# Performance work log

Hardware: AMD Instinct MI355X
Metric: run time of the kernel (lower is better)

The kernel has to match this reference:

```python
import jax, jax.numpy as jnp
import numpy as np

N = 50000        # nodes
E = 800000       # edges (avg degree 16)
IN = 128         # n_feat
C0, H0 = 32, 4   # layer0: out_channels, heads (concat -> 128)
C1, H1 = 32, 1   # layer1: out_channels, heads (mean)
NEG_SLOPE = 0.2


def setup_inputs() -> dict:
    key = jax.random.key(0)
    ks = jax.random.split(key, 16)
    def p(k, shape, fan):
        return jax.random.normal(k, shape, jnp.float32) / np.float32(np.sqrt(fan))
    x = jax.random.normal(ks[0], (N, IN), jnp.float32)
    edge_index = jax.random.randint(ks[1], (2, E), 0, N, dtype=jnp.int32)
    return {
        "x": x,
        "edge_index": edge_index,
        # layer 0 GATConv: in=128 -> 4 heads x 32, concat
        "W0": p(ks[2], (H0 * C0, IN), IN),
        "att_src0": p(ks[3], (H0, C0), C0),
        "att_dst0": p(ks[4], (H0, C0), C0),
        "bias0": jnp.zeros((H0 * C0,), jnp.float32),
        "linW0": p(ks[5], (H0 * C0, IN), IN),
        "linb0": jnp.zeros((H0 * C0,), jnp.float32),
        # layer 1 GATConv: in=128 -> 1 head x 32, mean
        "W1": p(ks[6], (H1 * C1, H0 * C0), H0 * C0),
        "att_src1": p(ks[7], (H1, C1), C1),
        "att_dst1": p(ks[8], (H1, C1), C1),
        "bias1": jnp.zeros((C1,), jnp.float32),
        "linW1": p(ks[9], (C1, H0 * C0), H0 * C0),
        "linb1": jnp.zeros((C1,), jnp.float32),
    }


def gat_conv(x, src, dst, W, att_src, att_dst, bias, concat):
    """PyG-style GATConv (self-loops already appended to src/dst)."""
    n = x.shape[0]
    H, C = att_src.shape
    h = (x @ W.T).reshape(n, H, C)                       # [N,H,C]
    a_src = jnp.einsum('nhc,hc->nh', h, att_src)          # [N,H]
    a_dst = jnp.einsum('nhc,hc->nh', h, att_dst)          # [N,H]
    e = jax.nn.leaky_relu(a_src[src] + a_dst[dst], NEG_SLOPE)  # [E,H]
    # segment softmax over incoming edges of each dst node
    m = jax.ops.segment_max(e, dst, num_segments=n)       # [N,H]
    ex = jnp.exp(e - m[dst])
    denom = jax.ops.segment_sum(ex, dst, num_segments=n)  # [N,H]
    alpha = ex / (denom[dst] + 1e-16)                     # [E,H]
    out = jax.ops.segment_sum(h[src] * alpha[:, :, None], dst, num_segments=n)  # [N,H,C]
    out = out.reshape(n, H * C) if concat else out.mean(axis=1)
    return out + bias


def reference(x, edge_index, W0, att_src0, att_dst0, bias0, linW0, linb0,
              W1, att_src1, att_dst1, bias1, linW1, linb1):
    n = x.shape[0]
    loop = jnp.arange(n, dtype=edge_index.dtype)
    src = jnp.concatenate([edge_index[0], loop])  # add self-loops
    dst = jnp.concatenate([edge_index[1], loop])
    # layer 0: conv + linear skip, then ELU (eval mode -> dropout is a no-op)
    h = gat_conv(x, src, dst, W0, att_src0, att_dst0, bias0, True) + x @ linW0.T + linb0
    h = jax.nn.elu(h)
    # layer 1 (last): conv + linear skip, no activation
    out = gat_conv(h, src, dst, W1, att_src1, att_dst1, bias1, False) + h @ linW1.T + linb1
    return out
```

## Files before the change

kernel.cpp:

```cpp
#include <hip/hip_runtime.h>
#include <hip/hip_bf16.h>


typedef __attribute__((ext_vector_type(8))) short bf8_t;
typedef __attribute__((ext_vector_type(4))) float f4_t;

#define NBUCK 256
#define BCAP  8192

__device__ inline short f2bf(float f) {
    return (short)__builtin_bit_cast(unsigned short, __float2bfloat16(f));
}
__device__ inline float blo(unsigned int p) { return __uint_as_float(p << 16); }
__device__ inline float bhi(unsigned int p) { return __uint_as_float(p & 0xffff0000u); }
__device__ inline float lrexp(float e) {
    e = (e > 0.f) ? e : 0.2f * e;
    return __expf(e);
}

__global__ void k_gz(int* __restrict__ gcur) {
    gcur[threadIdx.x] = threadIdx.x * BCAP;
}

__global__ __launch_bounds__(256) void k_initbucket(
    const int* __restrict__ ei,
    const float* __restrict__ W0, const float* __restrict__ lW0,
    const float* __restrict__ W1, const float* __restrict__ lW1,
    const float* __restrict__ b0, const float* __restrict__ lb0,
    const float* __restrict__ b1, const float* __restrict__ lb1,
    short* __restrict__ Wp0, short* __restrict__ lWp0,
    short* __restrict__ Wp1, short* __restrict__ lWp1,
    float* __restrict__ bc0, float* __restrict__ bc1,
    int* __restrict__ gcur,
    unsigned int* __restrict__ bucketed, int E, int T) {
    __shared__ int hist[NBUCK];
    __shared__ int gbase[NBUCK];
    int tid = threadIdx.x;

    if (blockIdx.x < 64) {
        int i = blockIdx.x * 256 + tid;
        {
            int j = i & 7, lane = (i >> 3) & 63, kc = i >> 9;
            int kb = kc & 3, ct = kc >> 2;
            int src = (ct * 16 + (lane & 15)) * 128 + kb * 32 + (lane >> 4) * 8 + j;
            Wp0[i]  = f2bf(W0[src]);
            lWp0[i] = f2bf(lW0[src]);
            if (i < 4096) {
                Wp1[i]  = f2bf(W1[src]);
                lWp1[i] = f2bf(lW1[src]);
            }
        }
        if (i < 128) bc0[i] = b0[i] + lb0[i];
        else if (i < 160) bc1[i - 128] = b1[i - 128] + lb1[i - 128];
        return;
    }

    int bb = blockIdx.x - 64;
    hist[tid] = 0;
    __syncthreads();
    int base = bb * 2048;
    unsigned int pk[8]; int rk[8]; int bk[8];
    #pragma unroll
    for (int j = 0; j < 8; j++) {
        int e = base + j * 256 + tid;
        if (e < T) {
            int src, dst;
            if (e < E) { src = ei[e]; dst = ei[E + e]; }
            else       { src = e - E; dst = src; }
            int b = dst >> 8;
            pk[j] = ((unsigned int)dst << 16) | (unsigned int)src;
            bk[j] = b;
            rk[j] = atomicAdd(&hist[b], 1);
        } else bk[j] = -1;
    }
    __syncthreads();
    int h = hist[tid];
    if (h > 0) gbase[tid] = atomicAdd(&gcur[tid], h);
    __syncthreads();
    #pragma unroll
    for (int j = 0; j < 8; j++)
        if (bk[j] >= 0)
            bucketed[gbase[bk[j]] + rk[j]] = pk[j];
}

__global__ void k_bscan(const int* __restrict__ gcur, int* __restrict__ bbase,
                        int* __restrict__ rowstart, int n) {
    __shared__ int buf[NBUCK];
    int t = threadIdx.x;
    int v = gcur[t] - t * BCAP;
    buf[t] = v;
    __syncthreads();
    for (int off = 1; off < NBUCK; off <<= 1) {
        int tv = (t >= off) ? buf[t - off] : 0;
        __syncthreads();
        buf[t] += tv;
        __syncthreads();
    }
    bbase[t] = buf[t] - v;
    if (t == NBUCK - 1) rowstart[n] = buf[t];
}


#define TSTR 136

__global__ __launch_bounds__(256) void k_fillgemm0(
    const unsigned int* __restrict__ bucketed, const int* __restrict__ gcur,
    const int* __restrict__ bbase, int* __restrict__ rowstart,
    unsigned short* __restrict__ esrc,
    const float* __restrict__ x,
    const short* __restrict__ Wp0, const short* __restrict__ lWp0,
    const float* __restrict__ as0, const float* __restrict__ ad0,
    __hip_bfloat16* __restrict__ h0, __hip_bfloat16* __restrict__ skipb,
    float* __restrict__ a0s, float* __restrict__ a0d, int N) {
    __shared__ int ihist[256];
    __shared__ int incl[256];
    __shared__ short tile[4][16 * TSTR];
    int NBK = (N + 255) >> 8;

    if ((int)blockIdx.x < NBK) {
        int b = blockIdx.x, t = threadIdx.x;
        int nodebase = b << 8;
        int used = gcur[b] - b * BCAP;
        const unsigned int* bk = bucketed + (size_t)b * BCAP;
        ihist[t] = 0;
        __syncthreads();
        for (int i = t; i < used; i += 256)
            atomicAdd(&ihist[(bk[i] >> 16) - nodebase], 1);
        __syncthreads();
        int v = ihist[t];
        incl[t] = v;
        __syncthreads();
        for (int off = 1; off < 256; off <<= 1) {
            int tv = (t >= off) ? incl[t - off] : 0;
            __syncthreads();
            incl[t] += tv;
            __syncthreads();
        }
        int myexcl = incl[t] - v;
        int rbase = bbase[b];
        int node = nodebase + t;
        if (node < N) rowstart[node] = rbase + myexcl;
        __syncthreads();
        ihist[t] = myexcl;
        __syncthreads();
        for (int i = t; i < used; i += 256) {
            unsigned int p = bk[i];
            int pos = atomicAdd(&ihist[(p >> 16) - nodebase], 1);
            esrc[rbase + pos] = (unsigned short)(p & 0xffffu);
        }
        return;
    }

    int bx = blockIdx.x - NBK;
    int wv = threadIdx.x >> 6, lane = threadIdx.x & 63;
    int rowbase = bx * 64 + wv * 16;
    int m = lane & 15, q = lane >> 4;
    int arow = rowbase + m; if (arow >= N) arow = N - 1;
    bf8_t a[4];
    #pragma unroll
    for (int kb = 0; kb < 4; kb++) {
        const float4* px = (const float4*)(x + (size_t)arow * 128 + kb * 32 + q * 8);
        float4 lo = px[0], hi = px[1];
        bf8_t f;
        f[0] = f2bf(lo.x); f[1] = f2bf(lo.y); f[2] = f2bf(lo.z); f[3] = f2bf(lo.w);
        f[4] = f2bf(hi.x); f[5] = f2bf(hi.y); f[6] = f2bf(hi.z); f[7] = f2bf(hi.w);
        a[kb] = f;
    }
    float sacc[4][4], dacc[4][4];
    #pragma unroll
    for (int h = 0; h < 4; h++)
        #pragma unroll
        for (int r = 0; r < 4; r++) { sacc[h][r] = 0.f; dacc[h][r] = 0.f; }
    short* tl = tile[wv];
    int r4 = lane >> 2, qt = lane & 3;
    int drow = rowbase + r4;

    #pragma unroll
    for (int ct = 0; ct < 8; ct++) {
        f4_t acc = {0.f, 0.f, 0.f, 0.f};
        #pragma unroll
        for (int kb = 0; kb < 4; kb++) {
            bf8_t b = *(const bf8_t*)(Wp0 + (((ct * 4 + kb) * 64 + lane) << 3));
            acc = __builtin_amdgcn_mfma_f32_16x16x32_bf16(a[kb], b, acc, 0, 0, 0);
        }
        int hd = ct >> 1;
        float ws = as0[ct * 16 + m], wd = ad0[ct * 16 + m];
        #pragma unroll
        for (int r = 0; r < 4; r++) {
            sacc[hd][r] += acc[r] * ws;
            dacc[hd][r] += acc[r] * wd;
            tl[(q * 4 + r) * TSTR + ct * 16 + m] = f2bf(acc[r]);
        }
    }
    if (drow < N) {
        short* dst = (short*)h0 + (size_t)drow * 128 + qt * 32;
        const short* srcp = tl + r4 * TSTR + qt * 32;
        #pragma unroll
        for (int s = 0; s < 4; s++)
            *(uint4*)(dst + s * 8) = *(const uint4*)(srcp + s * 8);
    }

    #pragma unroll
    for (int ct = 0; ct < 8; ct++) {
        f4_t acc = {0.f, 0.f, 0.f, 0.f};
        #pragma unroll
        for (int kb = 0; kb < 4; kb++) {
            bf8_t b = *(const bf8_t*)(lWp0 + (((ct * 4 + kb) * 64 + lane) << 3));
            acc = __builtin_amdgcn_mfma_f32_16x16x32_bf16(a[kb], b, acc, 0, 0, 0);
        }
        #pragma unroll
        for (int r = 0; r < 4; r++)
            tl[(q * 4 + r) * TSTR + ct * 16 + m] = f2bf(acc[r]);
    }
    if (drow < N) {
        short* dst = (short*)skipb + (size_t)drow * 128 + qt * 32;
        const short* srcp = tl + r4 * TSTR + qt * 32;
        #pragma unroll
        for (int s = 0; s < 4; s++)
            *(uint4*)(dst + s * 8) = *(const uint4*)(srcp + s * 8);
    }

    #pragma unroll
    for (int h = 0; h < 4; h++)
        #pragma unroll
        for (int r = 0; r < 4; r++) {
            float s = sacc[h][r], d = dacc[h][r];
            #pragma unroll
            for (int off = 1; off < 16; off <<= 1) {
                s += __shfl_xor(s, off);
                d += __shfl_xor(d, off);
            }
            sacc[h][r] = s; dacc[h][r] = d;
        }
    if (m < 4) {
        #pragma unroll
        for (int r = 0; r < 4; r++) {
            int row = rowbase + q * 4 + r;
            if (row < N) {
                float sv = (m == 0) ? sacc[0][r] : (m == 1) ? sacc[1][r]
                         : (m == 2) ? sacc[2][r] : sacc[3][r];
                float dv = (m == 0) ? dacc[0][r] : (m == 1) ? dacc[1][r]
                         : (m == 2) ? dacc[2][r] : dacc[3][r];
                a0s[row * 4 + m] = sv;
                a0d[row * 4 + m] = dv;
            }
        }
    }
}


__global__ __launch_bounds__(256) void k_gemm1(
    const __hip_bfloat16* __restrict__ hin,
    const short* __restrict__ Wp1, const short* __restrict__ lWp1,
    const float* __restrict__ as1, const float* __restrict__ ad1,
    __hip_bfloat16* __restrict__ h1, float* __restrict__ skipb ,
    float* __restrict__ a1s, float* __restrict__ a1d, int N) {
    __shared__ short th[4][16 * 40];
    __shared__ float ts[4][16 * 36];
    int wv = threadIdx.x >> 6, lane = threadIdx.x & 63;
    int rowbase = blockIdx.x * 64 + wv * 16;
    int m = lane & 15, q = lane >> 4;
    int arow = rowbase + m; if (arow >= N) arow = N - 1;
    const short* xs = (const short*)hin;
    bf8_t a[4];
    #pragma unroll
    for (int kb = 0; kb < 4; kb++)
        a[kb] = *(const bf8_t*)(xs + (size_t)arow * 128 + kb * 32 + q * 8);
    float sacc[4], dacc[4];
    #pragma unroll
    for (int r = 0; r < 4; r++) { sacc[r] = 0.f; dacc[r] = 0.f; }
    short* tlh = th[wv];
    float* tls = ts[wv];
    int r4 = lane >> 2, qt = lane & 3;
    int drow = rowbase + r4;

    #pragma unroll
    for (int ct = 0; ct < 2; ct++) {
        f4_t acc = {0.f, 0.f, 0.f, 0.f};
        #pragma unroll
        for (int kb = 0; kb < 4; kb++) {
            bf8_t b = *(const bf8_t*)(Wp1 + (((ct * 4 + kb) * 64 + lane) << 3));
            acc = __builtin_amdgcn_mfma_f32_16x16x32_bf16(a[kb], b, acc, 0, 0, 0);
        }
        float ws = as1[ct * 16 + m], wd = ad1[ct * 16 + m];
        #pragma unroll
        for (int r = 0; r < 4; r++) {
            sacc[r] += acc[r] * ws;
            dacc[r] += acc[r] * wd;
            tlh[(q * 4 + r) * 40 + ct * 16 + m] = f2bf(acc[r]);
        }
    }
    #pragma unroll
    for (int ct = 0; ct < 2; ct++) {
        f4_t acc = {0.f, 0.f, 0.f, 0.f};
        #pragma unroll
        for (int kb = 0; kb < 4; kb++) {
            bf8_t b = *(const bf8_t*)(lWp1 + (((ct * 4 + kb) * 64 + lane) << 3));
            acc = __builtin_amdgcn_mfma_f32_16x16x32_bf16(a[kb], b, acc, 0, 0, 0);
        }
        #pragma unroll
        for (int r = 0; r < 4; r++)
            tls[(q * 4 + r) * 36 + ct * 16 + m] = acc[r];
    }
    if (drow < N) {
        *(uint4*)((short*)h1 + (size_t)drow * 32 + qt * 8) =
            *(const uint4*)(tlh + r4 * 40 + qt * 8);
        float* dst = skipb + (size_t)drow * 32 + qt * 8;
        const float* srcp = tls + r4 * 36 + qt * 8;
        *(uint4*)(dst) = *(const uint4*)(srcp);
        *(uint4*)(dst + 4) = *(const uint4*)(srcp + 4);
    }
    #pragma unroll
    for (int r = 0; r < 4; r++) {
        float s = sacc[r], d = dacc[r];
        #pragma unroll
        for (int off = 1; off < 16; off <<= 1) {
            s += __shfl_xor(s, off);
            d += __shfl_xor(d, off);
        }
        if (m == 0) {
            int row = rowbase + q * 4 + r;
            if (row < N) { a1s[row] = s; a1d[row] = d; }
        }
    }
}


__global__ __launch_bounds__(256) void k_agg0(
    const int* __restrict__ rowstart, const unsigned short* __restrict__ esrc,
    const unsigned int* __restrict__ h0u,
    const float* __restrict__ a0s, const float* __restrict__ a0d,
    const float* __restrict__ bc0,
    unsigned int* __restrict__ h1in_u,
    int n) {
    int node = (blockIdx.x * 256 + threadIdx.x) >> 6;
    int lane = threadIdx.x & 63;
    if (node >= n) return;
    int g = lane >> 4, t = lane & 15, hd = t >> 2;
    float ad = a0d[node * 4 + hd];
    int s0 = rowstart[node], s1 = rowstart[node + 1];
    float den = 0.f;
    float acc[8];
    #pragma unroll
    for (int k = 0; k < 8; k++) acc[k] = 0.f;
    int i = s0 + g;
    for (; i + 12 < s1; i += 16) {
        int sE[4]; float e[4]; uint4 p[4];
        #pragma unroll
        for (int j = 0; j < 4; j++) sE[j] = esrc[i + 4 * j];
        #pragma unroll
        for (int j = 0; j < 4; j++) e[j] = a0s[sE[j] * 4 + hd] + ad;
        #pragma unroll
        for (int j = 0; j < 4; j++) p[j] = *(const uint4*)(h0u + (size_t)sE[j] * 64 + t * 4);
        #pragma unroll
        for (int j = 0; j < 4; j++) {
            float wgt = lrexp(e[j]);
            den += wgt;
            acc[0] += wgt * blo(p[j].x); acc[1] += wgt * bhi(p[j].x);
            acc[2] += wgt * blo(p[j].y); acc[3] += wgt * bhi(p[j].y);
            acc[4] += wgt * blo(p[j].z); acc[5] += wgt * bhi(p[j].z);
            acc[6] += wgt * blo(p[j].w); acc[7] += wgt * bhi(p[j].w);
        }
    }
    for (; i < s1; i += 4) {
        int s = esrc[i];
        float wv = lrexp(a0s[s * 4 + hd] + ad);
        uint4 p = *(const uint4*)(h0u + (size_t)s * 64 + t * 4);
        den += wv;
        acc[0] += wv * blo(p.x); acc[1] += wv * bhi(p.x);
        acc[2] += wv * blo(p.y); acc[3] += wv * bhi(p.y);
        acc[4] += wv * blo(p.z); acc[5] += wv * bhi(p.z);
        acc[6] += wv * blo(p.w); acc[7] += wv * bhi(p.w);
    }
    #pragma unroll
    for (int k = 0; k < 8; k++) {
        acc[k] += __shfl_xor(acc[k], 16);
        acc[k] += __shfl_xor(acc[k], 32);
    }
    den += __shfl_xor(den, 16);
    den += __shfl_xor(den, 32);
    if (g == 0) {
        float inv = 1.0f / (den + 1e-16f);
        uint4 sp = *(const uint4*)(h1in_u + (size_t)node * 64 + t * 4);
        int c0 = t * 8;
        float o[8];
        o[0] = acc[0] * inv + blo(sp.x) + bc0[c0 + 0];
        o[1] = acc[1] * inv + bhi(sp.x) + bc0[c0 + 1];
        o[2] = acc[2] * inv + blo(sp.y) + bc0[c0 + 2];
        o[3] = acc[3] * inv + bhi(sp.y) + bc0[c0 + 3];
        o[4] = acc[4] * inv + blo(sp.z) + bc0[c0 + 4];
        o[5] = acc[5] * inv + bhi(sp.z) + bc0[c0 + 5];
        o[6] = acc[6] * inv + blo(sp.w) + bc0[c0 + 6];
        o[7] = acc[7] * inv + bhi(sp.w) + bc0[c0 + 7];
        #pragma unroll
        for (int k = 0; k < 8; k++)
            o[k] = (o[k] > 0.f) ? o[k] : (__expf(o[k]) - 1.f);
        uint4 res;
        res.x = (unsigned int)(unsigned short)f2bf(o[0]) | ((unsigned int)(unsigned short)f2bf(o[1]) << 16);
        res.y = (unsigned int)(unsigned short)f2bf(o[2]) | ((unsigned int)(unsigned short)f2bf(o[3]) << 16);
        res.z = (unsigned int)(unsigned short)f2bf(o[4]) | ((unsigned int)(unsigned short)f2bf(o[5]) << 16);
        res.w = (unsigned int)(unsigned short)f2bf(o[6]) | ((unsigned int)(unsigned short)f2bf(o[7]) << 16);
        *(uint4*)(h1in_u + (size_t)node * 64 + t * 4) = res;
    }
}

__global__ __launch_bounds__(256) void k_agg1(
    const int* __restrict__ rowstart, const unsigned short* __restrict__ esrc,
    const __hip_bfloat16* __restrict__ h1,
    const float* __restrict__ a1s, const float* __restrict__ a1d,
    const float* __restrict__ bc1,
    float* __restrict__ out, int n) {
    int node = (blockIdx.x * 256 + threadIdx.x) >> 6;
    int lane = threadIdx.x & 63;
    if (node >= n) return;
    int g = lane >> 4, t = lane & 15;
    float ad = a1d[node];
    int s0 = rowstart[node], s1 = rowstart[node + 1];
    const unsigned int* h1w = (const unsigned int*)h1;
    float den = 0.f, acc0 = 0.f, acc1 = 0.f;
    int i = s0 + g;
    for (; i + 12 < s1; i += 16) {
        int sE[4]; float e[4]; unsigned int p[4];
        #pragma unroll
        for (int j = 0; j < 4; j++) sE[j] = esrc[i + 4 * j];
        #pragma unroll
        for (int j = 0; j < 4; j++) e[j] = a1s[sE[j]] + ad;
        #pragma unroll
        for (int j = 0; j < 4; j++) p[j] = h1w[(size_t)sE[j] * 16 + t];
        #pragma unroll
        for (int j = 0; j < 4; j++) {
            float wgt = lrexp(e[j]);
            den += wgt;
            acc0 += wgt * blo(p[j]);
            acc1 += wgt * bhi(p[j]);
        }
    }
    for (; i < s1; i += 4) {
        int s = esrc[i];
        float wv = lrexp(a1s[s] + ad);
        unsigned int p = h1w[(size_t)s * 16 + t];
        den += wv; acc0 += wv * blo(p); acc1 += wv * bhi(p);
    }
    acc0 += __shfl_xor(acc0, 16); acc0 += __shfl_xor(acc0, 32);
    acc1 += __shfl_xor(acc1, 16); acc1 += __shfl_xor(acc1, 32);
    den  += __shfl_xor(den, 16);  den  += __shfl_xor(den, 32);
    if (g == 0) {
        float inv = 1.0f / (den + 1e-16f);
        int c0 = t * 2;
        size_t idx = (size_t)node * 32 + c0;
        float2 sk = *(const float2*)(out + idx);
        float2 r;
        r.x = acc0 * inv + sk.x + bc1[c0];
        r.y = acc1 * inv + sk.y + bc1[c0 + 1];
        *(float2*)(out + idx) = r;
    }
}


extern "C" void kernel_launch(void* const* d_in, const int* in_sizes, int n_in,
                              void* d_out, int out_size, void* d_ws, size_t ws_size,
                              hipStream_t stream) {
    const float* x   = (const float*)d_in[0];
    const int*   ei  = (const int*)d_in[1];
    const float* W0  = (const float*)d_in[2];
    const float* as0 = (const float*)d_in[3];
    const float* ad0 = (const float*)d_in[4];
    const float* b0  = (const float*)d_in[5];
    const float* lW0 = (const float*)d_in[6];
    const float* lb0 = (const float*)d_in[7];
    const float* W1  = (const float*)d_in[8];
    const float* as1 = (const float*)d_in[9];
    const float* ad1 = (const float*)d_in[10];
    const float* b1  = (const float*)d_in[11];
    const float* lW1 = (const float*)d_in[12];
    const float* lb1 = (const float*)d_in[13];
    float* out = (float*)d_out;

    const int N = in_sizes[0] / 128;
    const int E = in_sizes[1] / 2;
    const int T = E + N;
    const int NBK  = (N + 255) >> 8;
    const int NBBK = (T + 2047) / 2048;

    char* w = (char*)d_ws;
    auto alloc = [&](size_t bytes) -> char* {
        char* p = w; w += (bytes + 255) / 256 * 256; return p;
    };
    int* rowstart  = (int*)alloc((size_t)(N + 1) * 4);
    int* gcur      = (int*)alloc(NBUCK * 4);
    int* bbase     = (int*)alloc(NBUCK * 4);
    unsigned int* bucketed = (unsigned int*)alloc((size_t)NBUCK * BCAP * 4);
    unsigned short* esrc = (unsigned short*)alloc((size_t)T * 2);
    float* aS      = (float*)alloc((size_t)N * 4 * 4);
    float* aD      = (float*)alloc((size_t)N * 4 * 4);
    __hip_bfloat16* hbuf = (__hip_bfloat16*)alloc((size_t)N * 128 * 2);
    __hip_bfloat16* h1in = (__hip_bfloat16*)alloc((size_t)N * 128 * 2);
    short* Wp0  = (short*)alloc(16384 * 2);
    short* lWp0 = (short*)alloc(16384 * 2);
    short* Wp1  = (short*)alloc(4096 * 2);
    short* lWp1 = (short*)alloc(4096 * 2);
    float* bc0  = (float*)alloc(128 * 4);
    float* bc1  = (float*)alloc(32 * 4);

    k_gz<<<1, NBUCK, 0, stream>>>(gcur);
    k_initbucket<<<64 + NBBK, 256, 0, stream>>>(ei, W0, lW0, W1, lW1,
                                                b0, lb0, b1, lb1,
                                                Wp0, lWp0, Wp1, lWp1, bc0, bc1,
                                                gcur, bucketed, E, T);
    k_bscan<<<1, NBUCK, 0, stream>>>(gcur, bbase, rowstart, N);
    k_fillgemm0<<<NBK + (N + 63) / 64, 256, 0, stream>>>(
        bucketed, gcur, bbase, rowstart, esrc,
        x, Wp0, lWp0, as0, ad0, hbuf, h1in, aS, aD, N);
    k_agg0<<<(N + 3) / 4, 256, 0, stream>>>(rowstart, esrc, (const unsigned int*)hbuf,
                                            aS, aD, bc0, (unsigned int*)h1in, N);
    k_gemm1<<<(N + 63) / 64, 256, 0, stream>>>(h1in, Wp1, lWp1, as1, ad1,
                                               hbuf, out, aS, aD, N);
    k_agg1<<<(N + 3) / 4, 256, 0, stream>>>(rowstart, esrc, hbuf, aS, aD,
                                            bc1, out, N);
}
```

Measured before the change: 210.5 us.

## Store layer-0 features as FP8 and fold bucket scan into fill kernel

Layer-0 projected features are converted to FP8 (e4m3) in the GEMM epilogue and unpacked with packed FP8-to-f32 conversions in the aggregation gather. This halves the bytes gathered per edge in the aggregation kernel, which is bound by random memory traffic. The separate single-block bucket-prefix-scan kernel is removed: every fill block recomputes the 256-entry scan itself, saving a launch at the cost of redundant work. FP8 storage lowers feature precision and may hurt accuracy against the tolerance.

```diff
diff --git a/kernel.cpp b/kernel.cpp
--- a/kernel.cpp
+++ b/kernel.cpp
@@ -4,6 +4,7 @@
 
 typedef __attribute__((ext_vector_type(8))) short bf8_t;
 typedef __attribute__((ext_vector_type(4))) float f4_t;
+typedef __attribute__((ext_vector_type(2))) float f2_t;
 
 #define NBUCK 256
 #define BCAP  8192
@@ -83,52 +84,29 @@
             bucketed[gbase[bk[j]] + rk[j]] = pk[j];
 }
 
-__global__ void k_bscan(const int* __restrict__ gcur, int* __restrict__ bbase,
-                        int* __restrict__ rowstart, int n) {
-    __shared__ int buf[NBUCK];
-    int t = threadIdx.x;
-    int v = gcur[t] - t * BCAP;
-    buf[t] = v;
-    __syncthreads();
-    for (int off = 1; off < NBUCK; off <<= 1) {
-        int tv = (t >= off) ? buf[t - off] : 0;
-        __syncthreads();
-        buf[t] += tv;
-        __syncthreads();
-    }
-    bbase[t] = buf[t] - v;
-    if (t == NBUCK - 1) rowstart[n] = buf[t];
-}
-
 
 #define TSTR 136
 
 __global__ __launch_bounds__(256) void k_fillgemm0(
     const unsigned int* __restrict__ bucketed, const int* __restrict__ gcur,
-    const int* __restrict__ bbase, int* __restrict__ rowstart,
+    int* __restrict__ rowstart,
     unsigned short* __restrict__ esrc,
     const float* __restrict__ x,
     const short* __restrict__ Wp0, const short* __restrict__ lWp0,
     const float* __restrict__ as0, const float* __restrict__ ad0,
-    __hip_bfloat16* __restrict__ h0, __hip_bfloat16* __restrict__ skipb,
+    unsigned char* __restrict__ h0f8, __hip_bfloat16* __restrict__ skipb,
     float* __restrict__ a0s, float* __restrict__ a0d, int N) {
     __shared__ int ihist[256];
     __shared__ int incl[256];
     __shared__ short tile[4][16 * TSTR];
+    __shared__ unsigned char t8[4][16 * 136];
     int NBK = (N + 255) >> 8;
 
     if ((int)blockIdx.x < NBK) {
         int b = blockIdx.x, t = threadIdx.x;
         int nodebase = b << 8;
-        int used = gcur[b] - b * BCAP;
-        const unsigned int* bk = bucketed + (size_t)b * BCAP;
-        ihist[t] = 0;
-        __syncthreads();
-        for (int i = t; i < used; i += 256)
-            atomicAdd(&ihist[(bk[i] >> 16) - nodebase], 1);
-        __syncthreads();
-        int v = ihist[t];
-        incl[t] = v;
+        int cntt = gcur[t] - t * BCAP;
+        incl[t] = cntt;
         __syncthreads();
         for (int off = 1; off < 256; off <<= 1) {
             int tv = (t >= off) ? incl[t - off] : 0;
@@ -136,8 +114,26 @@
             incl[t] += tv;
             __syncthreads();
         }
+        int rbase = (b > 0) ? incl[b - 1] : 0;
+        if (b == 0 && t == 255) rowstart[N] = incl[255];
+        int used = gcur[b] - b * BCAP;
+        const unsigned int* bk = bucketed + (size_t)b * BCAP;
+        __syncthreads();
+        ihist[t] = 0;
+        __syncthreads();
+        for (int i = t; i < used; i += 256)
+            atomicAdd(&ihist[(bk[i] >> 16) - nodebase], 1);
+        __syncthreads();
+        int v = ihist[t];
+        incl[t] = v;
+        __syncthreads();
+        for (int off = 1; off < 256; off <<= 1) {
+            int tv = (t >= off) ? incl[t - off] : 0;
+            __syncthreads();
+            incl[t] += tv;
+            __syncthreads();
+        }
         int myexcl = incl[t] - v;
-        int rbase = bbase[b];
         int node = nodebase + t;
         if (node < N) rowstart[node] = rbase + myexcl;
         __syncthreads();
@@ -172,6 +168,7 @@
         #pragma unroll
         for (int r = 0; r < 4; r++) { sacc[h][r] = 0.f; dacc[h][r] = 0.f; }
     short* tl = tile[wv];
+    unsigned char* t8l = t8[wv];
     int r4 = lane >> 2, qt = lane & 3;
     int drow = rowbase + r4;
 
@@ -189,15 +186,21 @@
         for (int r = 0; r < 4; r++) {
             sacc[hd][r] += acc[r] * ws;
             dacc[hd][r] += acc[r] * wd;
-            tl[(q * 4 + r) * TSTR + ct * 16 + m] = f2bf(acc[r]);
+            int pk8 = __builtin_amdgcn_cvt_pk_fp8_f32(acc[r], acc[r], 0, false);
+            t8l[(q * 4 + r) * 136 + ct * 16 + m] = (unsigned char)(pk8 & 0xff);
         }
     }
     if (drow < N) {
-        short* dst = (short*)h0 + (size_t)drow * 128 + qt * 32;
-        const short* srcp = tl + r4 * TSTR + qt * 32;
-        #pragma unroll
-        for (int s = 0; s < 4; s++)
-            *(uint4*)(dst + s * 8) = *(const uint4*)(srcp + s * 8);
+        const unsigned char* sp8 = t8l + r4 * 136 + qt * 32;
+        uint2 w0 = ((const uint2*)sp8)[0];
+        uint2 w1 = ((const uint2*)sp8)[1];
+        uint2 w2 = ((const uint2*)sp8)[2];
+        uint2 w3 = ((const uint2*)sp8)[3];
+        uint4 o0 = make_uint4(w0.x, w0.y, w1.x, w1.y);
+        uint4 o1 = make_uint4(w2.x, w2.y, w3.x, w3.y);
+        unsigned char* dst = h0f8 + (size_t)drow * 128 + qt * 32;
+        *(uint4*)dst = o0;
+        *(uint4*)(dst + 16) = o1;
     }
 
     #pragma unroll
@@ -328,7 +331,7 @@
 
 __global__ __launch_bounds__(256) void k_agg0(
     const int* __restrict__ rowstart, const unsigned short* __restrict__ esrc,
-    const unsigned int* __restrict__ h0u,
+    const uint2* __restrict__ h0f8,
     const float* __restrict__ a0s, const float* __restrict__ a0d,
     const float* __restrict__ bc0,
     unsigned int* __restrict__ h1in_u,
@@ -345,32 +348,40 @@
     for (int k = 0; k < 8; k++) acc[k] = 0.f;
     int i = s0 + g;
     for (; i + 12 < s1; i += 16) {
-        int sE[4]; float e[4]; uint4 p[4];
+        int sE[4]; float e[4]; uint2 p[4];
         #pragma unroll
         for (int j = 0; j < 4; j++) sE[j] = esrc[i + 4 * j];
         #pragma unroll
         for (int j = 0; j < 4; j++) e[j] = a0s[sE[j] * 4 + hd] + ad;
         #pragma unroll
-        for (int j = 0; j < 4; j++) p[j] = *(const uint4*)(h0u + (size_t)sE[j] * 64 + t * 4);
+        for (int j = 0; j < 4; j++) p[j] = h0f8[(size_t)sE[j] * 16 + t];
         #pragma unroll
         for (int j = 0; j < 4; j++) {
             float wgt = lrexp(e[j]);
             den += wgt;
-            acc[0] += wgt * blo(p[j].x); acc[1] += wgt * bhi(p[j].x);
-            acc[2] += wgt * blo(p[j].y); acc[3] += wgt * bhi(p[j].y);
-            acc[4] += wgt * blo(p[j].z); acc[5] += wgt * bhi(p[j].z);
-            acc[6] += wgt * blo(p[j].w); acc[7] += wgt * bhi(p[j].w);
+            f2_t c01 = __builtin_amdgcn_cvt_pk_f32_fp8(p[j].x, false);
+            f2_t c23 = __builtin_amdgcn_cvt_pk_f32_fp8(p[j].x, true);
+            f2_t c45 = __builtin_amdgcn_cvt_pk_f32_fp8(p[j].y, false);
+            f2_t c67 = __builtin_amdgcn_cvt_pk_f32_fp8(p[j].y, true);
+            acc[0] += wgt * c01.x; acc[1] += wgt * c01.y;
+            acc[2] += wgt * c23.x; acc[3] += wgt * c23.y;
+            acc[4] += wgt * c45.x; acc[5] += wgt * c45.y;
+            acc[6] += wgt * c67.x; acc[7] += wgt * c67.y;
         }
     }
     for (; i < s1; i += 4) {
         int s = esrc[i];
-        float wv = lrexp(a0s[s * 4 + hd] + ad);
-        uint4 p = *(const uint4*)(h0u + (size_t)s * 64 + t * 4);
-        den += wv;
-        acc[0] += wv * blo(p.x); acc[1] += wv * bhi(p.x);
-        acc[2] += wv * blo(p.y); acc[3] += wv * bhi(p.y);
-        acc[4] += wv * blo(p.z); acc[5] += wv * bhi(p.z);
-        acc[6] += wv * blo(p.w); acc[7] += wv * bhi(p.w);
+        float wgt = lrexp(a0s[s * 4 + hd] + ad);
+        uint2 p = h0f8[(size_t)s * 16 + t];
+        den += wgt;
+        f2_t c01 = __builtin_amdgcn_cvt_pk_f32_fp8(p.x, false);
+        f2_t c23 = __builtin_amdgcn_cvt_pk_f32_fp8(p.x, true);
+        f2_t c45 = __builtin_amdgcn_cvt_pk_f32_fp8(p.y, false);
+        f2_t c67 = __builtin_amdgcn_cvt_pk_f32_fp8(p.y, true);
+        acc[0] += wgt * c01.x; acc[1] += wgt * c01.y;
+        acc[2] += wgt * c23.x; acc[3] += wgt * c23.y;
+        acc[4] += wgt * c45.x; acc[5] += wgt * c45.y;
+        acc[6] += wgt * c67.x; acc[7] += wgt * c67.y;
     }
     #pragma unroll
     for (int k = 0; k < 8; k++) {
@@ -488,12 +499,11 @@
     };
     int* rowstart  = (int*)alloc((size_t)(N + 1) * 4);
     int* gcur      = (int*)alloc(NBUCK * 4);
-    int* bbase     = (int*)alloc(NBUCK * 4);
     unsigned int* bucketed = (unsigned int*)alloc((size_t)NBUCK * BCAP * 4);
     unsigned short* esrc = (unsigned short*)alloc((size_t)T * 2);
     float* aS      = (float*)alloc((size_t)N * 4 * 4);
     float* aD      = (float*)alloc((size_t)N * 4 * 4);
-    __hip_bfloat16* hbuf = (__hip_bfloat16*)alloc((size_t)N * 128 * 2);
+    char* hbuf     = alloc((size_t)N * 128 * 2);
     __hip_bfloat16* h1in = (__hip_bfloat16*)alloc((size_t)N * 128 * 2);
     short* Wp0  = (short*)alloc(16384 * 2);
     short* lWp0 = (short*)alloc(16384 * 2);
@@ -507,14 +517,13 @@
                                                 b0, lb0, b1, lb1,
                                                 Wp0, lWp0, Wp1, lWp1, bc0, bc1,
                                                 gcur, bucketed, E, T);
-    k_bscan<<<1, NBUCK, 0, stream>>>(gcur, bbase, rowstart, N);
     k_fillgemm0<<<NBK + (N + 63) / 64, 256, 0, stream>>>(
-        bucketed, gcur, bbase, rowstart, esrc,
-        x, Wp0, lWp0, as0, ad0, hbuf, h1in, aS, aD, N);
-    k_agg0<<<(N + 3) / 4, 256, 0, stream>>>(rowstart, esrc, (const unsigned int*)hbuf,
+        bucketed, gcur, rowstart, esrc,
+        x, Wp0, lWp0, as0, ad0, (unsigned char*)hbuf, h1in, aS, aD, N);
+    k_agg0<<<(N + 3) / 4, 256, 0, stream>>>(rowstart, esrc, (const uint2*)hbuf,
                                             aS, aD, bc0, (unsigned int*)h1in, N);
     k_gemm1<<<(N + 63) / 64, 256, 0, stream>>>(h1in, Wp1, lWp1, as1, ad1,
-                                               hbuf, out, aS, aD, N);
-    k_agg1<<<(N + 3) / 4, 256, 0, stream>>>(rowstart, esrc, hbuf, aS, aD,
-                                            bc1, out, N);
-}
+                                               (__hip_bfloat16*)hbuf, out, aS, aD, N);
+    k_agg1<<<(N + 3) / 4, 256, 0, stream>>>(rowstart, esrc, (const __hip_bfloat16*)hbuf,
+                                            aS, aD, bc1, out, N);
+}
```

After: 202.3 us. 3.9% less time.
